# Optimization experiments

Measured on AMD Instinct MI355X. Metric: run time of the kernel, lower is better.

## Reference

```python
import jax, jax.numpy as jnp
import numpy as np

B, N, H, L, V = 512, 48, 256, 64, 800  # trees, nodes/tree (chain), hidden, latent, vocab


def _build_structure():
    # Chain tree: nodes 0..N-1; edges per tree: 2i=(i->i+1), 2i+1=(i+1->i).
    # DFS order with reverse edges: forward steps t=0..N-2 (label 0), then backtrack (label 1).
    T = 2 * (N - 1)
    Et = 2 * (N - 1)
    eid = np.zeros(T, np.int32); pred = np.zeros(T, np.int32); pm = np.zeros(T, bool)
    vl = np.zeros(T, np.int32)
    in0 = np.zeros(T, np.int32); m0 = np.zeros(T, bool)
    in1 = np.zeros(T, np.int32); m1 = np.zeros(T, bool)
    lab = np.zeros(T, np.int32)
    for t in range(N - 1):  # forward: edge (t -> t+1)
        eid[t] = 2 * t
        if t > 0:
            pred[t], pm[t] = 2 * (t - 1), True  # line-graph pred (t-1 -> t)
        v = t + 1; vl[t] = v
        in0[t], m0[t] = 2 * (v - 1), True       # in-edge (v-1 -> v)
        if v < N - 1:
            in1[t], m1[t] = 2 * v + 1, True     # in-edge (v+1 -> v), m still zero here
        lab[t] = 0
    for k in range(N - 1):  # backtrack: edge (u -> u-1)
        t = N - 1 + k; u = N - 1 - k
        eid[t] = 2 * (u - 1) + 1
        if u < N - 1:
            pred[t], pm[t] = 2 * u + 1, True    # line-graph pred (u+1 -> u)
        v = u - 1; vl[t] = v
        if v > 0:
            in0[t], m0[t] = 2 * (v - 1), True
        in1[t], m1[t] = 2 * v + 1, True
        lab[t] = 1
    eoff = (np.arange(B, dtype=np.int32) * Et)[None, :]
    noff = (np.arange(B, dtype=np.int32) * N)[None, :]
    src_l = np.empty(Et, np.int32); dst_l = np.empty(Et, np.int32)
    for i in range(N - 1):
        src_l[2 * i], dst_l[2 * i] = i, i + 1
        src_l[2 * i + 1], dst_l[2 * i + 1] = i + 1, i
    d = dict(
        step_eid=eid[:, None] + eoff,
        step_pred=pred[:, None] + eoff,
        step_pmask=np.broadcast_to(pm[:, None], (T, B)).copy(),
        step_v=vl[:, None] + noff,
        step_in0=in0[:, None] + eoff,
        step_m0=np.broadcast_to(m0[:, None], (T, B)).copy(),
        step_in1=in1[:, None] + eoff,
        step_m1=np.broadcast_to(m1[:, None], (T, B)).copy(),
        step_label=lab,
        edge_src=(src_l[None, :] + (np.arange(B, dtype=np.int32) * N)[:, None]).reshape(-1),
        edge_dst=(dst_l[None, :] + (np.arange(B, dtype=np.int32) * N)[:, None]).reshape(-1),
        root_ids=np.arange(B, dtype=np.int32) * N,
    )
    return {k: jnp.asarray(v) for k, v in d.items()}


def setup_inputs() -> dict:
    key = jax.random.key(0)
    ks = jax.random.split(key, 20)
    lin = lambda k, i, o: jax.random.normal(k, (i, o), jnp.float32) * (1.0 / np.sqrt(i))
    inp = _build_structure()
    inp['wid'] = jax.random.randint(ks[0], (B * N,), 0, V)
    inp['tree_vec'] = jax.random.normal(ks[1], (B, L), jnp.float32)
    inp['embedding'] = jax.random.normal(ks[2], (V, H), jnp.float32) * 0.1
    inp['Wz'] = lin(ks[3], 2 * H, H); inp['bz'] = jnp.zeros((H,), jnp.float32)
    inp['Wr'] = lin(ks[4], H, H)                                   # no bias (W_r)
    inp['Ur'] = lin(ks[5], H, H); inp['br'] = jnp.zeros((H,), jnp.float32)
    inp['Wh'] = lin(ks[6], 2 * H, H); inp['bh'] = jnp.zeros((H,), jnp.float32)
    inp['W_w'] = lin(ks[7], H + L, H); inp['W_b'] = jnp.zeros((H,), jnp.float32)
    inp['U_w'] = lin(ks[8], 2 * H + L, H); inp['U_b'] = jnp.zeros((H,), jnp.float32)
    inp['Wo_w'] = lin(ks[9], H, V); inp['Wo_b'] = jnp.zeros((V,), jnp.float32)
    inp['Us_w'] = lin(ks[10], H, 1); inp['Us_b'] = jnp.zeros((1,), jnp.float32)
    inp['n_fwd'] = N - 1
    return inp


def reference(wid, tree_vec, embedding, Wz, bz, Wr, Ur, br, Wh, bh,
              W_w, W_b, U_w, U_b, Wo_w, Wo_b, Us_w, Us_b,
              edge_src, edge_dst, root_ids,
              step_eid, step_pred, step_pmask, step_v,
              step_in0, step_m0, step_in1, step_m1,
              step_label, n_fwd):
    Hd = embedding.shape[1]
    Bn, Ld = tree_vec.shape
    E = edge_src.shape[0]
    x = embedding[wid]          # [n_nodes, H]
    src_x = x[edge_src]         # [E, H]
    dst_x = x[edge_dst]

    def gru_step(carry, st):
        m, rm = carry
        e = st['eid']
        pm = st['pmask'][:, None]
        s = jnp.where(pm, m[st['pred']], 0.0)        # line-graph pull of m -> s
        arm = jnp.where(pm, rm[st['pred']], 0.0)     # pull of rm -> accum_rm
        sx = src_x[e]
        z = jax.nn.sigmoid(jnp.concatenate([sx, s], 1) @ Wz + bz)
        mt = jnp.tanh(jnp.concatenate([sx, arm], 1) @ Wh + bh)
        m_e = (1.0 - z) * s + z * mt
        r = jax.nn.sigmoid(dst_x[e] @ Wr + m_e @ Ur + br)
        m = m.at[e].set(m_e)
        rm = rm.at[e].set(r * m_e)
        # node pull: h[v] = sum of m over all in-edges of v
        h_v = jnp.where(st['m0'][:, None], m[st['in0']], 0.0) \
            + jnp.where(st['m1'][:, None], m[st['in1']], 0.0)
        return (m, rm), h_v

    xs = {'eid': step_eid, 'pred': step_pred, 'pmask': step_pmask,
          'in0': step_in0, 'm0': step_m0, 'in1': step_in1, 'm1': step_m1}
    init = (jnp.zeros((E, Hd), x.dtype), jnp.zeros((E, Hd), x.dtype))
    _, hs = jax.lax.scan(gru_step, init, xs)  # [T, B, H]

    T = step_eid.shape[0]
    x_v = x[step_v]                                   # [T, B, H]
    tv = jnp.broadcast_to(tree_vec, (T, Bn, Ld))
    h_root = jnp.zeros((1, Bn, Hd), x.dtype)
    x_root = x[root_ids][None]
    p_in = jnp.concatenate([
        jnp.concatenate([x_root, h_root, tree_vec[None]], -1),
        jnp.concatenate([x_v, hs, tv], -1)], 0).reshape((T + 1) * Bn, 2 * Hd + Ld)
    p_tgt = jnp.concatenate([
        jnp.repeat((1 - step_label).astype(jnp.float32), Bn),
        jnp.zeros((Bn,), jnp.float32)])

    q_in = jnp.concatenate([
        jnp.concatenate([h_root[0], tree_vec], -1)[None],
        jnp.concatenate([hs[:n_fwd], tv[:n_fwd]], -1)], 0).reshape((n_fwd + 1) * Bn, Hd + Ld)
    q_tgt = jnp.concatenate([wid[root_ids][None], wid[step_v[:n_fwd]]], 0).reshape(-1)

    q = jax.nn.relu(q_in @ W_w + W_b) @ Wo_w + Wo_b
    p = (jax.nn.relu(p_in @ U_w + U_b) @ Us_w + Us_b)[:, 0]

    nt = jnp.float32(Bn)
    p_loss = jnp.sum(jnp.maximum(p, 0.0) - p * p_tgt + jnp.log1p(jnp.exp(-jnp.abs(p)))) / nt
    logq = jax.nn.log_softmax(q, -1)
    q_loss = -jnp.sum(jnp.take_along_axis(logq, q_tgt[:, None], 1)) / nt
    p_acc = jnp.mean(((p > 0).astype(jnp.int32) == p_tgt.astype(jnp.int32)).astype(jnp.float32))
    q_acc = jnp.mean((jnp.argmax(q, 1) == q_tgt).astype(jnp.float32))
    return q_loss, p_loss, q_acc, p_acc
```

## Files before the change

### kernel.cpp

```cpp
#include <hip/hip_runtime.h>
#include <math.h>

#define NTREE 512
#define NNODE 48
#define HD 256
#define LD 64
#define VOC 800
#define TSTEP 94
#define NFWD 47

typedef __attribute__((ext_vector_type(8))) short s8v;
typedef __attribute__((ext_vector_type(4))) float f4v;

__device__ __forceinline__ float sigm(float x) { return 1.f / (1.f + expf(-x)); }
__device__ __forceinline__ float sigm_f(float x) {
    return __builtin_amdgcn_rcpf(1.f + __expf(-x));
}
__device__ __forceinline__ float tanh_f(float x) {
    return 1.f - 2.f * __builtin_amdgcn_rcpf(1.f + __expf(2.f * x));
}

__device__ __forceinline__ float bfu(unsigned short u) {
    union { unsigned int i; float f; } c; c.i = ((unsigned int)u) << 16; return c.f;
}
__device__ __forceinline__ unsigned short f2bf(float f) {
    union { float f; unsigned int u; } c; c.f = f;
    return (unsigned short)((c.u + 0x7fffu + ((c.u >> 16) & 1u)) >> 16);
}
__device__ __forceinline__ s8v frag(const unsigned short* p) {
    union { int4 i; s8v v; } u; u.i = *(const int4*)p; return u.v;
}
__device__ __forceinline__ s8v zfrag() {
    union { int4 i; s8v v; } u; u.i = make_int4(0, 0, 0, 0); return u.v;
}
__device__ __forceinline__ void pin(s8v& v) {
    asm volatile("" : "+v"(v));
}
__device__ __forceinline__ void bar_lgkm() {
    asm volatile("s_waitcnt lgkmcnt(0)\n\ts_barrier" ::: "memory");
}

#define PV 8
__global__ __launch_bounds__(256) void prep_xproj(
    const float* __restrict__ emb,
    const float* __restrict__ Wz, const float* __restrict__ bz,
    const float* __restrict__ Wh, const float* __restrict__ bh,
    const float* __restrict__ Wr, const float* __restrict__ br,
    float* __restrict__ xzT, float* __restrict__ xhT, float* __restrict__ xrT)
{
    __shared__ float embL[PV][HD];
    const int j = threadIdx.x;
    const int v0 = blockIdx.x * PV;
    for (int r = 0; r < PV; ++r) embL[r][j] = emb[(v0 + r) * HD + j];
    __syncthreads();

    float az[PV], ah[PV], ar[PV];
#pragma unroll
    for (int r = 0; r < PV; ++r) { az[r] = bz[j]; ah[r] = bh[j]; ar[r] = br[j]; }
    for (int i = 0; i < HD; i += 4) {
        float wz0 = Wz[(i + 0) * HD + j], wz1 = Wz[(i + 1) * HD + j];
        float wz2 = Wz[(i + 2) * HD + j], wz3 = Wz[(i + 3) * HD + j];
        float wh0 = Wh[(i + 0) * HD + j], wh1 = Wh[(i + 1) * HD + j];
        float wh2 = Wh[(i + 2) * HD + j], wh3 = Wh[(i + 3) * HD + j];
        float wr0 = Wr[(i + 0) * HD + j], wr1 = Wr[(i + 1) * HD + j];
        float wr2 = Wr[(i + 2) * HD + j], wr3 = Wr[(i + 3) * HD + j];
#pragma unroll
        for (int r = 0; r < PV; ++r) {
            float4 e = *(const float4*)&embL[r][i];
            az[r] += e.x * wz0 + e.y * wz1 + e.z * wz2 + e.w * wz3;
            ah[r] += e.x * wh0 + e.y * wh1 + e.z * wh2 + e.w * wh3;
            ar[r] += e.x * wr0 + e.y * wr1 + e.z * wr2 + e.w * wr3;
        }
    }
#pragma unroll
    for (int r = 0; r < PV; ++r) {
        xzT[(v0 + r) * HD + j] = az[r];
        xhT[(v0 + r) * HD + j] = ah[r];
        xrT[(v0 + r) * HD + j] = ar[r];
    }
}

__global__ __launch_bounds__(256) void tcvt3(
    const float* __restrict__ Wz, const float* __restrict__ Wh,
    const float* __restrict__ Ur,
    unsigned short* __restrict__ WzT, unsigned short* __restrict__ WhT,
    unsigned short* __restrict__ UrT)
{
    const int which = blockIdx.x >> 8, n = blockIdx.x & 255, k = threadIdx.x;
    const float* src = (which == 0) ? (Wz + HD * HD) : (which == 1) ? (Wh + HD * HD) : Ur;
    unsigned short* dst = (which == 0) ? WzT : (which == 1) ? WhT : UrT;
    dst[n * HD + k] = f2bf(src[k * HD + n]);
}

__global__ __launch_bounds__(256) void tcvtQ(
    const float* __restrict__ Ww, const float* __restrict__ Wow,
    const float* __restrict__ Uw,
    unsigned short* __restrict__ W1T, unsigned short* __restrict__ WoT,
    unsigned short* __restrict__ UwT)
{
    int b = blockIdx.x;
    if (b < 256) {
        for (int k = threadIdx.x; k < 320; k += 256)
            W1T[b * 320 + k] = f2bf(Ww[k * 256 + b]);
    } else if (b < 1056) {
        int n = b - 256;
        WoT[n * 256 + threadIdx.x] = f2bf(Wow[threadIdx.x * VOC + n]);
    } else {
        int n = b - 1056;
        for (int k = threadIdx.x; k < 576; k += 256)
            UwT[n * 576 + k] = f2bf(Uw[k * 256 + n]);
    }
}

__global__ __launch_bounds__(256) void cvtE(
    const float* __restrict__ emb, const float* __restrict__ tv,
    unsigned short* __restrict__ embB, unsigned short* __restrict__ tvB)
{
    int idx = blockIdx.x * 256 + threadIdx.x;
    if (idx < VOC * HD) embB[idx] = f2bf(emb[idx]);
    else {
        int i2 = idx - VOC * HD;
        if (i2 < NTREE * LD) tvB[i2] = f2bf(tv[i2]);
    }
}

__global__ __launch_bounds__(512, 2) void gru10(
    const int* __restrict__ wid,
    const float* __restrict__ xzT, const float* __restrict__ xhT,
    const float* __restrict__ xrT,
    const unsigned short* __restrict__ WzT, const unsigned short* __restrict__ WhT,
    const unsigned short* __restrict__ UrT,
    unsigned short* __restrict__ hsb)
{
    __shared__ unsigned short urL[16 * 8 * 64 * 8];
    __shared__ unsigned short mBL[2][2][HD], armBL[2][2][HD];
    __shared__ int widL[2][NNODE];

    const int tid = threadIdx.x;
    const int wave = tid >> 6, lane = tid & 63;
    const int lq = lane >> 4, ln = lane & 15;
    const int b0 = blockIdx.x * 2;
    const int T0 = 2 * wave, T1 = T0 + 1;
    const int ftree = lane >> 5;
    const int fcol  = wave * 32 + (lane & 31);
    const int srcl  = lane & 15;
    const bool hi16 = (lane & 16) != 0;
    const bool hi32 = (lane & 32) != 0;

    if (tid < 2 * NNODE) widL[tid / NNODE][tid % NNODE] =
        wid[(b0 + tid / NNODE) * NNODE + (tid % NNODE)];

#pragma unroll
    for (int s = 0; s < 16; ++s) {
        *(int4*)&urL[((s * 8 + wave) * 64 + lane) * 8] =
            *(const int4*)&UrT[(s * 16 + ln) * HD + wave * 32 + lq * 8];
    }

    s8v wz0[8], wz1[8], wh0[8], wh1[8];
#pragma unroll
    for (int kt = 0; kt < 8; ++kt) {
        const int ko = kt * 32 + lq * 8;
        wz0[kt] = frag(&WzT[(T0 * 16 + ln) * HD + ko]);
        wz1[kt] = frag(&WzT[(T1 * 16 + ln) * HD + ko]);
        wh0[kt] = frag(&WhT[(T0 * 16 + ln) * HD + ko]);
        wh1[kt] = frag(&WhT[(T1 * 16 + ln) * HD + ko]);
    }
#pragma unroll
    for (int kt = 0; kt < 8; ++kt) {
        pin(wz0[kt]); pin(wz1[kt]); pin(wh0[kt]); pin(wh1[kt]);
    }
    __syncthreads();

    float cxz, cxh, cxr, chsp = 0.f, me = 0.f;
    float nxz = 0.f, nxh = 0.f, nxr = 0.f, nhsp = 0.f;
    {
        const int ws = widL[ftree][0], wd = widL[ftree][1];
        cxz = xzT[ws * HD + fcol];
        cxh = xhT[ws * HD + fcol];
        cxr = xrT[wd * HD + fcol];
    }

#pragma unroll 2
    for (int t = 0; t < TSTEP; ++t) {
        const int par = t & 1, nxt = par ^ 1;
        const bool fwd = t < NFWD;
        const bool hp = (t != 0) && (t != NFWD);

        {
            if (t == NFWD)
                chsp = bfu(hsb[((NFWD - 2) * NTREE + b0 + ftree) * HD + fcol]);
            const int tn = t + 1;
            if (tn < TSTEP) {
                const bool fwdn = tn < NFWD;
                const int un = TSTEP - tn;
                const int srcn = fwdn ? tn : un;
                const int dstn = fwdn ? (tn + 1) : (un - 1);
                const int ws = widL[ftree][srcn], wd = widL[ftree][dstn];
                nxz = xzT[ws * HD + fcol];
                nxh = xhT[ws * HD + fcol];
                nxr = xrT[wd * HD + fcol];
                nhsp = 0.f;
                if (tn > NFWD && dstn > 0)
                    nhsp = bfu(hsb[((dstn - 1) * NTREE + b0 + ftree) * HD + fcol]);
            }
        }

        float az = 0.f, ah = 0.f;
        if (hp) {
            f4v cz0 = (f4v){0.f,0.f,0.f,0.f}, cz1 = cz0, ch0 = cz0, ch1 = cz0;
#pragma unroll
            for (int kt = 0; kt < 8; ++kt) {
                const int ko = kt * 32 + lq * 8;
                s8v am = (ln < 2) ? frag(&mBL[par][ln][ko]) : zfrag();
                s8v aa = (ln < 2) ? frag(&armBL[par][ln][ko]) : zfrag();
                cz0 = __builtin_amdgcn_mfma_f32_16x16x32_bf16(am, wz0[kt], cz0, 0, 0, 0);
                cz1 = __builtin_amdgcn_mfma_f32_16x16x32_bf16(am, wz1[kt], cz1, 0, 0, 0);
                ch0 = __builtin_amdgcn_mfma_f32_16x16x32_bf16(aa, wh0[kt], ch0, 0, 0, 0);
                ch1 = __builtin_amdgcn_mfma_f32_16x16x32_bf16(aa, wh1[kt], ch1, 0, 0, 0);
            }
            float a00 = __shfl(cz0[0], srcl), a01 = __shfl(cz0[1], srcl);
            float a10 = __shfl(cz1[0], srcl), a11 = __shfl(cz1[1], srcl);
            az = hi16 ? (hi32 ? a11 : a10) : (hi32 ? a01 : a00);
            float h00 = __shfl(ch0[0], srcl), h01 = __shfl(ch0[1], srcl);
            float h10 = __shfl(ch1[0], srcl), h11 = __shfl(ch1[1], srcl);
            ah = hi16 ? (hi32 ? h11 : h10) : (hi32 ? h01 : h00);
        }

        {
            float azv = cxz, ahv = cxh, sold = 0.f;
            if (hp) { azv += az; ahv += ah; sold = me; }
            float z = sigm_f(azv), mt = tanh_f(ahv);
            me = sold + z * (mt - sold);
            float hv = fwd ? me : (me + chsp);
            hsb[(t * NTREE + b0 + ftree) * HD + fcol] = f2bf(hv);
            mBL[nxt][ftree][fcol] = f2bf(me);
        }
        bar_lgkm();

        {
            f4v cr0 = (f4v){0.f,0.f,0.f,0.f}, cr1 = cr0;
#pragma unroll
            for (int kt = 0; kt < 8; ++kt) {
                const int ko = kt * 32 + lq * 8;
                s8v a = (ln < 2) ? frag(&mBL[nxt][ln][ko]) : zfrag();
                s8v b0f = frag(&urL[((T0 * 8 + kt) * 64 + lane) * 8]);
                s8v b1f = frag(&urL[((T1 * 8 + kt) * 64 + lane) * 8]);
                cr0 = __builtin_amdgcn_mfma_f32_16x16x32_bf16(a, b0f, cr0, 0, 0, 0);
                cr1 = __builtin_amdgcn_mfma_f32_16x16x32_bf16(a, b1f, cr1, 0, 0, 0);
            }
            float r00 = __shfl(cr0[0], srcl), r01 = __shfl(cr0[1], srcl);
            float r10 = __shfl(cr1[0], srcl), r11 = __shfl(cr1[1], srcl);
            float ar = hi16 ? (hi32 ? r11 : r10) : (hi32 ? r01 : r00);
            float r = sigm_f(cxr + ar);
            armBL[nxt][ftree][fcol] = f2bf(r * me);
            cxz = nxz; cxh = nxh; cxr = nxr; chsp = nhsp;
        }
        bar_lgkm();
    }
}

#define QG 32
#define PG 32
struct QSmem {
    unsigned short X1L[QG][328];
    unsigned short hidL[QG][264];
    int tgts[QG];
    float wred[4][QG][4];
};
struct PSmem {
    unsigned short XL[PG][584];
    int widL[PG];
    float wredp[4][PG];
};

__global__ __launch_bounds__(256) void heads(
    const int* __restrict__ wid,
    const unsigned short* __restrict__ tvB,
    const unsigned short* __restrict__ embB,
    const unsigned short* __restrict__ hsb,
    const unsigned short* __restrict__ W1T,
    const unsigned short* __restrict__ WoT,
    const unsigned short* __restrict__ UwT,
    const float* __restrict__ Wb, const float* __restrict__ Wob,
    const float* __restrict__ Ub,
    const float* __restrict__ Usw, const float* __restrict__ Usb,
    float* __restrict__ acc)
{
    __shared__ __align__(16) char smem[sizeof(QSmem) > sizeof(PSmem) ? sizeof(QSmem) : sizeof(PSmem)];
    const int tid = threadIdx.x;
    const int wave = tid >> 6, lane = tid & 63;
    const int lq = lane >> 4, ln = lane & 15;

    if (blockIdx.x < 768) {
        QSmem& S = *(QSmem*)smem;
        const int trow = blockIdx.x >> 4;
        const int b0 = (blockIdx.x & 15) * QG;

        if (tid < QG) S.tgts[tid] = wid[(b0 + tid) * NNODE + trow];
        if (trow == 0) {
            int4 z = make_int4(0, 0, 0, 0);
            for (int idx = tid; idx < QG * 32; idx += 256) {
                int m = idx >> 5, c = idx & 31;
                *(int4*)&S.X1L[m][c * 8] = z;
            }
        } else {
            const unsigned short* hrow = hsb + (size_t)(trow - 1) * NTREE * HD;
            for (int idx = tid; idx < QG * 32; idx += 256) {
                int m = idx >> 5, c = idx & 31;
                *(int4*)&S.X1L[m][c * 8] = *(const int4*)&hrow[(b0 + m) * HD + c * 8];
            }
        }
        for (int idx = tid; idx < QG * 8; idx += 256) {
            int m = idx >> 3, c = idx & 7;
            *(int4*)&S.X1L[m][256 + c * 8] = *(const int4*)&tvB[(b0 + m) * LD + c * 8];
        }
        __syncthreads();

        f4v acc1[2][4];
#pragma unroll
        for (int mt = 0; mt < 2; ++mt)
#pragma unroll
            for (int nt = 0; nt < 4; ++nt) acc1[mt][nt] = (f4v){0.f, 0.f, 0.f, 0.f};
#pragma unroll
        for (int kt = 0; kt < 10; ++kt) {
            s8v a0 = frag(&S.X1L[ln][kt * 32 + lq * 8]);
            s8v a1 = frag(&S.X1L[16 + ln][kt * 32 + lq * 8]);
#pragma unroll
            for (int nt = 0; nt < 4; ++nt) {
                int n = wave * 64 + nt * 16 + ln;
                s8v b = frag(&W1T[n * 320 + kt * 32 + lq * 8]);
                acc1[0][nt] = __builtin_amdgcn_mfma_f32_16x16x32_bf16(a0, b, acc1[0][nt], 0, 0, 0);
                acc1[1][nt] = __builtin_amdgcn_mfma_f32_16x16x32_bf16(a1, b, acc1[1][nt], 0, 0, 0);
            }
        }
#pragma unroll
        for (int nt = 0; nt < 4; ++nt) {
            int col = wave * 64 + nt * 16 + ln;
            float wb = Wb[col];
#pragma unroll
            for (int mt = 0; mt < 2; ++mt)
#pragma unroll
                for (int r = 0; r < 4; ++r)
                    S.hidL[mt * 16 + lq * 4 + r][col] = f2bf(fmaxf(acc1[mt][nt][r] + wb, 0.f));
        }
        __syncthreads();

        int rt[2][4];
#pragma unroll
        for (int mt = 0; mt < 2; ++mt)
#pragma unroll
            for (int r = 0; r < 4; ++r) rt[mt][r] = S.tgts[mt * 16 + lq * 4 + r];
        float mx[2][4], ls[2][4], tg[2][4]; int am[2][4];
#pragma unroll
        for (int mt = 0; mt < 2; ++mt)
#pragma unroll
            for (int r = 0; r < 4; ++r) { mx[mt][r] = -1e30f; ls[mt][r] = 0.f; tg[mt][r] = 0.f; am[mt][r] = 1 << 30; }

        for (int nt = wave; nt < 50; nt += 4) {
            int n = nt * 16 + ln;
            const unsigned short* wrow = WoT + n * 256;
            f4v a2[2];
            a2[0] = (f4v){0.f, 0.f, 0.f, 0.f}; a2[1] = (f4v){0.f, 0.f, 0.f, 0.f};
#pragma unroll
            for (int kt = 0; kt < 8; ++kt) {
                s8v a0 = frag(&S.hidL[ln][kt * 32 + lq * 8]);
                s8v a1 = frag(&S.hidL[16 + ln][kt * 32 + lq * 8]);
                s8v b = frag(&wrow[kt * 32 + lq * 8]);
                a2[0] = __builtin_amdgcn_mfma_f32_16x16x32_bf16(a0, b, a2[0], 0, 0, 0);
                a2[1] = __builtin_amdgcn_mfma_f32_16x16x32_bf16(a1, b, a2[1], 0, 0, 0);
            }
            float bias = Wob[n];
#pragma unroll
            for (int mt = 0; mt < 2; ++mt)
#pragma unroll
                for (int r = 0; r < 4; ++r) {
                    float v = a2[mt][r] + bias;
                    if (n == rt[mt][r]) tg[mt][r] = v;
                    float nm = fmaxf(mx[mt][r], v);
                    ls[mt][r] = ls[mt][r] * __expf(mx[mt][r] - nm) + __expf(v - nm);
                    if (v > mx[mt][r]) am[mt][r] = n;
                    mx[mt][r] = nm;
                }
        }

#pragma unroll
        for (int s = 1; s < 16; s <<= 1) {
#pragma unroll
            for (int mt = 0; mt < 2; ++mt)
#pragma unroll
                for (int r = 0; r < 4; ++r) {
                    float mo = __shfl_xor(mx[mt][r], s);
                    float lo = __shfl_xor(ls[mt][r], s);
                    int   ao = __shfl_xor(am[mt][r], s);
                    float to = __shfl_xor(tg[mt][r], s);
                    tg[mt][r] += to;
                    float nm = fmaxf(mx[mt][r], mo);
                    ls[mt][r] = ls[mt][r] * __expf(mx[mt][r] - nm) + lo * __expf(mo - nm);
                    if (mo > mx[mt][r] || (mo == mx[mt][r] && ao < am[mt][r])) am[mt][r] = ao;
                    mx[mt][r] = nm;
                }
        }
        if (ln == 0) {
#pragma unroll
            for (int mt = 0; mt < 2; ++mt)
#pragma unroll
                for (int r = 0; r < 4; ++r) {
                    int row = mt * 16 + lq * 4 + r;
                    S.wred[wave][row][0] = mx[mt][r];
                    S.wred[wave][row][1] = ls[mt][r];
                    S.wred[wave][row][2] = __int_as_float(am[mt][r]);
                    S.wred[wave][row][3] = tg[mt][r];
                }
        }
        __syncthreads();

        float lossv = 0.f, corrv = 0.f;
        if (tid < QG) {
            float m_ = -1e30f, l_ = 0.f, t_ = 0.f; int a_ = 1 << 30;
#pragma unroll
            for (int w = 0; w < 4; ++w) {
                float mo = S.wred[w][tid][0], lo = S.wred[w][tid][1], to = S.wred[w][tid][3];
                int ao = __float_as_int(S.wred[w][tid][2]);
                t_ += to;
                float nm = fmaxf(m_, mo);
                l_ = l_ * __expf(m_ - nm) + lo * __expf(mo - nm);
                if (mo > m_ || (mo == m_ && ao < a_)) a_ = ao;
                m_ = nm;
            }
            lossv = m_ + logf(l_) - t_;
            corrv = (a_ == S.tgts[tid]) ? 1.f : 0.f;
        }
        if (wave == 0) {
            for (int s = 32; s; s >>= 1) {
                lossv += __shfl_down(lossv, s);
                corrv += __shfl_down(corrv, s);
            }
            if (tid == 0) {
                int slot = blockIdx.x & 255;
                atomicAdd(&acc[0 * 256 + slot], lossv);
                atomicAdd(&acc[2 * 256 + slot], corrv);
            }
        }
    } else {
        PSmem& S = *(PSmem*)smem;
        const int pb = blockIdx.x - 768;
        const int trow = pb >> 4;
        const int b0 = (pb & 15) * PG;
        const int node = (trow == 0) ? 0 : ((trow <= NFWD) ? trow : (TSTEP - trow));

        if (tid < PG) S.widL[tid] = wid[(b0 + tid) * NNODE + node];
        __syncthreads();

        for (int idx = tid; idx < PG * 32; idx += 256) {
            int m = idx >> 5, c = idx & 31;
            *(int4*)&S.XL[m][c * 8] = *(const int4*)&embB[S.widL[m] * HD + c * 8];
        }
        if (trow == 0) {
            int4 z = make_int4(0, 0, 0, 0);
            for (int idx = tid; idx < PG * 32; idx += 256) {
                int m = idx >> 5, c = idx & 31;
                *(int4*)&S.XL[m][256 + c * 8] = z;
            }
        } else {
            const unsigned short* hrow = hsb + (size_t)(trow - 1) * NTREE * HD;
            for (int idx = tid; idx < PG * 32; idx += 256) {
                int m = idx >> 5, c = idx & 31;
                *(int4*)&S.XL[m][256 + c * 8] = *(const int4*)&hrow[(b0 + m) * HD + c * 8];
            }
        }
        for (int idx = tid; idx < PG * 8; idx += 256) {
            int m = idx >> 3, c = idx & 7;
            *(int4*)&S.XL[m][512 + c * 8] = *(const int4*)&tvB[(b0 + m) * LD + c * 8];
        }
        __syncthreads();

        f4v a1[2][4];
#pragma unroll
        for (int mt = 0; mt < 2; ++mt)
#pragma unroll
            for (int nt = 0; nt < 4; ++nt) a1[mt][nt] = (f4v){0.f, 0.f, 0.f, 0.f};
        for (int kt = 0; kt < 18; ++kt) {
            s8v a0 = frag(&S.XL[ln][kt * 32 + lq * 8]);
            s8v am_ = frag(&S.XL[16 + ln][kt * 32 + lq * 8]);
#pragma unroll
            for (int nt = 0; nt < 4; ++nt) {
                int n = wave * 64 + nt * 16 + ln;
                s8v b = frag(&UwT[n * 576 + kt * 32 + lq * 8]);
                a1[0][nt] = __builtin_amdgcn_mfma_f32_16x16x32_bf16(a0, b, a1[0][nt], 0, 0, 0);
                a1[1][nt] = __builtin_amdgcn_mfma_f32_16x16x32_bf16(am_, b, a1[1][nt], 0, 0, 0);
            }
        }
        float part[2][4] = {{0, 0, 0, 0}, {0, 0, 0, 0}};
#pragma unroll
        for (int nt = 0; nt < 4; ++nt) {
            int n = wave * 64 + nt * 16 + ln;
            float ub = Ub[n], us = Usw[n];
#pragma unroll
            for (int mt = 0; mt < 2; ++mt)
#pragma unroll
                for (int r = 0; r < 4; ++r)
                    part[mt][r] += fmaxf(a1[mt][nt][r] + ub, 0.f) * us;
        }
#pragma unroll
        for (int s = 1; s < 16; s <<= 1) {
#pragma unroll
            for (int mt = 0; mt < 2; ++mt)
#pragma unroll
                for (int r = 0; r < 4; ++r)
                    part[mt][r] += __shfl_xor(part[mt][r], s);
        }
        if (ln == 0) {
#pragma unroll
            for (int mt = 0; mt < 2; ++mt)
#pragma unroll
                for (int r = 0; r < 4; ++r)
                    S.wredp[wave][mt * 16 + lq * 4 + r] = part[mt][r];
        }
        __syncthreads();

        float lossv = 0.f, corrv = 0.f;
        if (tid < PG) {
            float p = S.wredp[0][tid] + S.wredp[1][tid] + S.wredp[2][tid] + S.wredp[3][tid] + Usb[0];
            float tgt = (trow < NFWD) ? 1.f : 0.f;
            lossv = fmaxf(p, 0.f) - p * tgt + log1pf(expf(-fabsf(p)));
            corrv = (((p > 0.f) ? 1 : 0) == ((trow < NFWD) ? 1 : 0)) ? 1.f : 0.f;
        }
        if (wave == 0) {
            for (int s = 32; s; s >>= 1) {
                lossv += __shfl_down(lossv, s);
                corrv += __shfl_down(corrv, s);
            }
            if (tid == 0) {
                int slot = blockIdx.x & 255;
                atomicAdd(&acc[1 * 256 + slot], lossv);
                atomicAdd(&acc[3 * 256 + slot], corrv);
            }
        }
    }
}

__global__ void init_kernel(float* __restrict__ acc) {
    acc[threadIdx.x] = 0.f;
}

__global__ void fin_kernel(const float* __restrict__ acc, float* __restrict__ out) {
    const int tid = threadIdx.x;
    const int c = tid >> 6, lane = tid & 63;
    float v = 0.f;
    for (int i = lane; i < 256; i += 64) v += acc[c * 256 + i];
    for (int s = 32; s; s >>= 1) v += __shfl_down(v, s);
    if (lane == 0) {
        const float sc[4] = {1.f / 512.f, 1.f / 512.f, 1.f / 24576.f, 1.f / 48640.f};
        out[c] = v * sc[c];
    }
}

extern "C" void kernel_launch(void* const* d_in, const int* in_sizes, int n_in,
                              void* d_out, int out_size, void* d_ws, size_t ws_size,
                              hipStream_t stream) {
    const int*   wid  = (const int*)  d_in[12];
    const float* tv   = (const float*)d_in[13];
    const float* emb  = (const float*)d_in[14];
    const float* Wz   = (const float*)d_in[15];
    const float* bz   = (const float*)d_in[16];
    const float* Wr   = (const float*)d_in[17];
    const float* Ur   = (const float*)d_in[18];
    const float* br   = (const float*)d_in[19];
    const float* Wh   = (const float*)d_in[20];
    const float* bh   = (const float*)d_in[21];
    const float* Ww   = (const float*)d_in[22];
    const float* Wb   = (const float*)d_in[23];
    const float* Uw   = (const float*)d_in[24];
    const float* Ubias= (const float*)d_in[25];
    const float* Wow  = (const float*)d_in[26];
    const float* Wob  = (const float*)d_in[27];
    const float* Usw  = (const float*)d_in[28];
    const float* Usb  = (const float*)d_in[29];

    char* w = (char*)d_ws;
    float* accb = (float*)w;
    float* xzT  = (float*)(w + 4096);
    float* xhT  = (float*)(w + 823296);
    float* xrT  = (float*)(w + 1642496);
    unsigned short* WzT2 = (unsigned short*)(w + 2461696);
    unsigned short* WhT2 = (unsigned short*)(w + 2592768);
    unsigned short* UrT2 = (unsigned short*)(w + 2723840);
    unsigned short* hsb  = (unsigned short*)(w + 2854912);
    unsigned short* W1T  = (unsigned short*)(w + 27496448);
    unsigned short* WoT  = (unsigned short*)(w + 27660288);
    unsigned short* UwT  = (unsigned short*)(w + 28069888);
    unsigned short* embB = (unsigned short*)(w + 28364800);
    unsigned short* tvB  = (unsigned short*)(w + 28774400);

    init_kernel<<<1, 1024, 0, stream>>>(accb);
    prep_xproj<<<VOC / PV, 256, 0, stream>>>(emb, Wz, bz, Wh, bh, Wr, br, xzT, xhT, xrT);
    tcvt3<<<768, 256, 0, stream>>>(Wz, Wh, Ur, WzT2, WhT2, UrT2);
    tcvtQ<<<1312, 256, 0, stream>>>(Ww, Wow, Uw, W1T, WoT, UwT);
    cvtE<<<(VOC * HD + NTREE * LD + 255) / 256, 256, 0, stream>>>(emb, tv, embB, tvB);
    gru10<<<NTREE / 2, 512, 0, stream>>>(wid, xzT, xhT, xrT, WzT2, WhT2, UrT2, hsb);
    heads<<<768 + 1520, 256, 0, stream>>>(wid, tvB, embB, hsb, W1T, WoT, UwT,
                                          Wb, Wob, Ubias, Usw, Usb, accb);
    fin_kernel<<<1, 256, 0, stream>>>(accb, (float*)d_out);
}
```

Baseline: 455.3 us.

## Merge prep kernels, split MFMA accumulator chains, load head operands directly

```diff
diff --git a/kernel.cpp b/kernel.cpp
--- a/kernel.cpp
+++ b/kernel.cpp
@@ -12,7 +12,6 @@
 typedef __attribute__((ext_vector_type(8))) short s8v;
 typedef __attribute__((ext_vector_type(4))) float f4v;
 
-__device__ __forceinline__ float sigm(float x) { return 1.f / (1.f + expf(-x)); }
 __device__ __forceinline__ float sigm_f(float x) {
     return __builtin_amdgcn_rcpf(1.f + __expf(-x));
 }
@@ -32,9 +31,6 @@
 }
 __device__ __forceinline__ s8v zfrag() {
     union { int4 i; s8v v; } u; u.i = make_int4(0, 0, 0, 0); return u.v;
-}
-__device__ __forceinline__ void pin(s8v& v) {
-    asm volatile("" : "+v"(v));
 }
 __device__ __forceinline__ void bar_lgkm() {
     asm volatile("s_waitcnt lgkmcnt(0)\n\ts_barrier" ::: "memory");
@@ -80,51 +76,52 @@
     }
 }
 
-__global__ __launch_bounds__(256) void tcvt3(
+__global__ __launch_bounds__(256) void prep_misc(
     const float* __restrict__ Wz, const float* __restrict__ Wh,
     const float* __restrict__ Ur,
-    unsigned short* __restrict__ WzT, unsigned short* __restrict__ WhT,
-    unsigned short* __restrict__ UrT)
-{
-    const int which = blockIdx.x >> 8, n = blockIdx.x & 255, k = threadIdx.x;
-    const float* src = (which == 0) ? (Wz + HD * HD) : (which == 1) ? (Wh + HD * HD) : Ur;
-    unsigned short* dst = (which == 0) ? WzT : (which == 1) ? WhT : UrT;
-    dst[n * HD + k] = f2bf(src[k * HD + n]);
-}
-
-__global__ __launch_bounds__(256) void tcvtQ(
     const float* __restrict__ Ww, const float* __restrict__ Wow,
     const float* __restrict__ Uw,
+    const float* __restrict__ emb, const float* __restrict__ tv,
+    unsigned short* __restrict__ WzT, unsigned short* __restrict__ WhT,
+    unsigned short* __restrict__ UrT,
     unsigned short* __restrict__ W1T, unsigned short* __restrict__ WoT,
-    unsigned short* __restrict__ UwT)
+    unsigned short* __restrict__ UwT,
+    unsigned short* __restrict__ embB, unsigned short* __restrict__ tvB,
+    float* __restrict__ acc)
 {
     int b = blockIdx.x;
-    if (b < 256) {
-        for (int k = threadIdx.x; k < 320; k += 256)
-            W1T[b * 320 + k] = f2bf(Ww[k * 256 + b]);
-    } else if (b < 1056) {
-        int n = b - 256;
-        WoT[n * 256 + threadIdx.x] = f2bf(Wow[threadIdx.x * VOC + n]);
+    if (b < 4) {
+        acc[b * 256 + threadIdx.x] = 0.f;
+    } else if (b < 772) {
+        int bb = b - 4;
+        const int which = bb >> 8, n = bb & 255, k = threadIdx.x;
+        const float* src = (which == 0) ? (Wz + HD * HD) : (which == 1) ? (Wh + HD * HD) : Ur;
+        unsigned short* dst = (which == 0) ? WzT : (which == 1) ? WhT : UrT;
+        dst[n * HD + k] = f2bf(src[k * HD + n]);
+    } else if (b < 2084) {
+        int bb = b - 772;
+        if (bb < 256) {
+            for (int k = threadIdx.x; k < 320; k += 256)
+                W1T[bb * 320 + k] = f2bf(Ww[k * 256 + bb]);
+        } else if (bb < 1056) {
+            int n = bb - 256;
+            WoT[n * 256 + threadIdx.x] = f2bf(Wow[threadIdx.x * VOC + n]);
+        } else {
+            int n = bb - 1056;
+            for (int k = threadIdx.x; k < 576; k += 256)
+                UwT[n * 576 + k] = f2bf(Uw[k * 256 + n]);
+        }
     } else {
-        int n = b - 1056;
-        for (int k = threadIdx.x; k < 576; k += 256)
-            UwT[n * 576 + k] = f2bf(Uw[k * 256 + n]);
-    }
-}
-
-__global__ __launch_bounds__(256) void cvtE(
-    const float* __restrict__ emb, const float* __restrict__ tv,
-    unsigned short* __restrict__ embB, unsigned short* __restrict__ tvB)
-{
-    int idx = blockIdx.x * 256 + threadIdx.x;
-    if (idx < VOC * HD) embB[idx] = f2bf(emb[idx]);
-    else {
-        int i2 = idx - VOC * HD;
-        if (i2 < NTREE * LD) tvB[i2] = f2bf(tv[i2]);
-    }
-}
-
-__global__ __launch_bounds__(512, 2) void gru10(
+        int idx = (b - 2084) * 256 + threadIdx.x;
+        if (idx < VOC * HD) embB[idx] = f2bf(emb[idx]);
+        else {
+            int i2 = idx - VOC * HD;
+            if (i2 < NTREE * LD) tvB[i2] = f2bf(tv[i2]);
+        }
+    }
+}
+
+__global__ __launch_bounds__(512, 2) void gru11(
     const int* __restrict__ wid,
     const float* __restrict__ xzT, const float* __restrict__ xhT,
     const float* __restrict__ xrT,
@@ -164,10 +161,6 @@
         wz1[kt] = frag(&WzT[(T1 * 16 + ln) * HD + ko]);
         wh0[kt] = frag(&WhT[(T0 * 16 + ln) * HD + ko]);
         wh1[kt] = frag(&WhT[(T1 * 16 + ln) * HD + ko]);
-    }
-#pragma unroll
-    for (int kt = 0; kt < 8; ++kt) {
-        pin(wz0[kt]); pin(wz1[kt]); pin(wh0[kt]); pin(wh1[kt]);
     }
     __syncthreads();
 
@@ -207,17 +200,30 @@
 
         float az = 0.f, ah = 0.f;
         if (hp) {
-            f4v cz0 = (f4v){0.f,0.f,0.f,0.f}, cz1 = cz0, ch0 = cz0, ch1 = cz0;
-#pragma unroll
-            for (int kt = 0; kt < 8; ++kt) {
+            f4v cz0a = (f4v){0.f,0.f,0.f,0.f}, cz0b = cz0a, cz1a = cz0a, cz1b = cz0a;
+            f4v ch0a = cz0a, ch0b = cz0a, ch1a = cz0a, ch1b = cz0a;
+#pragma unroll
+            for (int kt = 0; kt < 4; ++kt) {
                 const int ko = kt * 32 + lq * 8;
                 s8v am = (ln < 2) ? frag(&mBL[par][ln][ko]) : zfrag();
                 s8v aa = (ln < 2) ? frag(&armBL[par][ln][ko]) : zfrag();
-                cz0 = __builtin_amdgcn_mfma_f32_16x16x32_bf16(am, wz0[kt], cz0, 0, 0, 0);
-                cz1 = __builtin_amdgcn_mfma_f32_16x16x32_bf16(am, wz1[kt], cz1, 0, 0, 0);
-                ch0 = __builtin_amdgcn_mfma_f32_16x16x32_bf16(aa, wh0[kt], ch0, 0, 0, 0);
-                ch1 = __builtin_amdgcn_mfma_f32_16x16x32_bf16(aa, wh1[kt], ch1, 0, 0, 0);
-            }
+                cz0a = __builtin_amdgcn_mfma_f32_16x16x32_bf16(am, wz0[kt], cz0a, 0, 0, 0);
+                cz1a = __builtin_amdgcn_mfma_f32_16x16x32_bf16(am, wz1[kt], cz1a, 0, 0, 0);
+                ch0a = __builtin_amdgcn_mfma_f32_16x16x32_bf16(aa, wh0[kt], ch0a, 0, 0, 0);
+                ch1a = __builtin_amdgcn_mfma_f32_16x16x32_bf16(aa, wh1[kt], ch1a, 0, 0, 0);
+            }
+#pragma unroll
+            for (int kt = 4; kt < 8; ++kt) {
+                const int ko = kt * 32 + lq * 8;
+                s8v am = (ln < 2) ? frag(&mBL[par][ln][ko]) : zfrag();
+                s8v aa = (ln < 2) ? frag(&armBL[par][ln][ko]) : zfrag();
+                cz0b = __builtin_amdgcn_mfma_f32_16x16x32_bf16(am, wz0[kt], cz0b, 0, 0, 0);
+                cz1b = __builtin_amdgcn_mfma_f32_16x16x32_bf16(am, wz1[kt], cz1b, 0, 0, 0);
+                ch0b = __builtin_amdgcn_mfma_f32_16x16x32_bf16(aa, wh0[kt], ch0b, 0, 0, 0);
+                ch1b = __builtin_amdgcn_mfma_f32_16x16x32_bf16(aa, wh1[kt], ch1b, 0, 0, 0);
+            }
+            f4v cz0 = cz0a + cz0b, cz1 = cz1a + cz1b;
+            f4v ch0 = ch0a + ch0b, ch1 = ch1a + ch1b;
             float a00 = __shfl(cz0[0], srcl), a01 = __shfl(cz0[1], srcl);
             float a10 = __shfl(cz1[0], srcl), a11 = __shfl(cz1[1], srcl);
             az = hi16 ? (hi32 ? a11 : a10) : (hi32 ? a01 : a00);
@@ -238,16 +244,26 @@
         bar_lgkm();
 
         {
-            f4v cr0 = (f4v){0.f,0.f,0.f,0.f}, cr1 = cr0;
-#pragma unroll
-            for (int kt = 0; kt < 8; ++kt) {
+            f4v cr0a = (f4v){0.f,0.f,0.f,0.f}, cr0b = cr0a, cr1a = cr0a, cr1b = cr0a;
+#pragma unroll
+            for (int kt = 0; kt < 4; ++kt) {
                 const int ko = kt * 32 + lq * 8;
                 s8v a = (ln < 2) ? frag(&mBL[nxt][ln][ko]) : zfrag();
                 s8v b0f = frag(&urL[((T0 * 8 + kt) * 64 + lane) * 8]);
                 s8v b1f = frag(&urL[((T1 * 8 + kt) * 64 + lane) * 8]);
-                cr0 = __builtin_amdgcn_mfma_f32_16x16x32_bf16(a, b0f, cr0, 0, 0, 0);
-                cr1 = __builtin_amdgcn_mfma_f32_16x16x32_bf16(a, b1f, cr1, 0, 0, 0);
-            }
+                cr0a = __builtin_amdgcn_mfma_f32_16x16x32_bf16(a, b0f, cr0a, 0, 0, 0);
+                cr1a = __builtin_amdgcn_mfma_f32_16x16x32_bf16(a, b1f, cr1a, 0, 0, 0);
+            }
+#pragma unroll
+            for (int kt = 4; kt < 8; ++kt) {
+                const int ko = kt * 32 + lq * 8;
+                s8v a = (ln < 2) ? frag(&mBL[nxt][ln][ko]) : zfrag();
+                s8v b0f = frag(&urL[((T0 * 8 + kt) * 64 + lane) * 8]);
+                s8v b1f = frag(&urL[((T1 * 8 + kt) * 64 + lane) * 8]);
+                cr0b = __builtin_amdgcn_mfma_f32_16x16x32_bf16(a, b0f, cr0b, 0, 0, 0);
+                cr1b = __builtin_amdgcn_mfma_f32_16x16x32_bf16(a, b1f, cr1b, 0, 0, 0);
+            }
+            f4v cr0 = cr0a + cr0b, cr1 = cr1a + cr1b;
             float r00 = __shfl(cr0[0], srcl), r01 = __shfl(cr0[1], srcl);
             float r10 = __shfl(cr1[0], srcl), r11 = __shfl(cr1[1], srcl);
             float ar = hi16 ? (hi32 ? r11 : r10) : (hi32 ? r01 : r00);
@@ -262,13 +278,11 @@
 #define QG 32
 #define PG 32
 struct QSmem {
-    unsigned short X1L[QG][328];
     unsigned short hidL[QG][264];
     int tgts[QG];
     float wred[4][QG][4];
 };
 struct PSmem {
-    unsigned short XL[PG][584];
     int widL[PG];
     float wredp[4][PG];
 };
@@ -297,34 +311,26 @@
         const int b0 = (blockIdx.x & 15) * QG;
 
         if (tid < QG) S.tgts[tid] = wid[(b0 + tid) * NNODE + trow];
-        if (trow == 0) {
-            int4 z = make_int4(0, 0, 0, 0);
-            for (int idx = tid; idx < QG * 32; idx += 256) {
-                int m = idx >> 5, c = idx & 31;
-                *(int4*)&S.X1L[m][c * 8] = z;
-            }
-        } else {
-            const unsigned short* hrow = hsb + (size_t)(trow - 1) * NTREE * HD;
-            for (int idx = tid; idx < QG * 32; idx += 256) {
-                int m = idx >> 5, c = idx & 31;
-                *(int4*)&S.X1L[m][c * 8] = *(const int4*)&hrow[(b0 + m) * HD + c * 8];
-            }
-        }
-        for (int idx = tid; idx < QG * 8; idx += 256) {
-            int m = idx >> 3, c = idx & 7;
-            *(int4*)&S.X1L[m][256 + c * 8] = *(const int4*)&tvB[(b0 + m) * LD + c * 8];
-        }
-        __syncthreads();
 
         f4v acc1[2][4];
 #pragma unroll
         for (int mt = 0; mt < 2; ++mt)
 #pragma unroll
             for (int nt = 0; nt < 4; ++nt) acc1[mt][nt] = (f4v){0.f, 0.f, 0.f, 0.f};
+        const unsigned short* hrow = hsb + (size_t)(trow - 1) * NTREE * HD;
 #pragma unroll
         for (int kt = 0; kt < 10; ++kt) {
-            s8v a0 = frag(&S.X1L[ln][kt * 32 + lq * 8]);
-            s8v a1 = frag(&S.X1L[16 + ln][kt * 32 + lq * 8]);
+            s8v a0, a1;
+            if (kt < 8) {
+                if (trow == 0) { a0 = zfrag(); a1 = zfrag(); }
+                else {
+                    a0 = frag(&hrow[(b0 + ln) * HD + kt * 32 + lq * 8]);
+                    a1 = frag(&hrow[(b0 + 16 + ln) * HD + kt * 32 + lq * 8]);
+                }
+            } else {
+                a0 = frag(&tvB[(b0 + ln) * LD + (kt - 8) * 32 + lq * 8]);
+                a1 = frag(&tvB[(b0 + 16 + ln) * LD + (kt - 8) * 32 + lq * 8]);
+            }
 #pragma unroll
             for (int nt = 0; nt < 4; ++nt) {
                 int n = wave * 64 + nt * 16 + ln;
@@ -345,6 +351,13 @@
         }
         __syncthreads();
 
+        s8v ha0[8], ha1[8];
+#pragma unroll
+        for (int kt = 0; kt < 8; ++kt) {
+            ha0[kt] = frag(&S.hidL[ln][kt * 32 + lq * 8]);
+            ha1[kt] = frag(&S.hidL[16 + ln][kt * 32 + lq * 8]);
+        }
+
         int rt[2][4];
 #pragma unroll
         for (int mt = 0; mt < 2; ++mt)
@@ -363,11 +376,9 @@
             a2[0] = (f4v){0.f, 0.f, 0.f, 0.f}; a2[1] = (f4v){0.f, 0.f, 0.f, 0.f};
 #pragma unroll
             for (int kt = 0; kt < 8; ++kt) {
-                s8v a0 = frag(&S.hidL[ln][kt * 32 + lq * 8]);
-                s8v a1 = frag(&S.hidL[16 + ln][kt * 32 + lq * 8]);
                 s8v b = frag(&wrow[kt * 32 + lq * 8]);
-                a2[0] = __builtin_amdgcn_mfma_f32_16x16x32_bf16(a0, b, a2[0], 0, 0, 0);
-                a2[1] = __builtin_amdgcn_mfma_f32_16x16x32_bf16(a1, b, a2[1], 0, 0, 0);
+                a2[0] = __builtin_amdgcn_mfma_f32_16x16x32_bf16(ha0[kt], b, a2[0], 0, 0, 0);
+                a2[1] = __builtin_amdgcn_mfma_f32_16x16x32_bf16(ha1[kt], b, a2[1], 0, 0, 0);
             }
             float bias = Wob[n];
 #pragma unroll
@@ -376,10 +387,11 @@
                 for (int r = 0; r < 4; ++r) {
                     float v = a2[mt][r] + bias;
                     if (n == rt[mt][r]) tg[mt][r] = v;
-                    float nm = fmaxf(mx[mt][r], v);
-                    ls[mt][r] = ls[mt][r] * __expf(mx[mt][r] - nm) + __expf(v - nm);
-                    if (v > mx[mt][r]) am[mt][r] = n;
-                    mx[mt][r] = nm;
+                    float d = v - mx[mt][r];
+                    float e = __expf(-fabsf(d));
+                    bool newmax = d > 0.f;
+                    ls[mt][r] = fmaf(ls[mt][r], newmax ? e : 1.f, newmax ? 1.f : e);
+                    if (newmax) { mx[mt][r] = v; am[mt][r] = n; }
                 }
         }
 
@@ -450,38 +462,30 @@
 
         if (tid < PG) S.widL[tid] = wid[(b0 + tid) * NNODE + node];
         __syncthreads();
-
-        for (int idx = tid; idx < PG * 32; idx += 256) {
-            int m = idx >> 5, c = idx & 31;
-            *(int4*)&S.XL[m][c * 8] = *(const int4*)&embB[S.widL[m] * HD + c * 8];
-        }
-        if (trow == 0) {
-            int4 z = make_int4(0, 0, 0, 0);
-            for (int idx = tid; idx < PG * 32; idx += 256) {
-                int m = idx >> 5, c = idx & 31;
-                *(int4*)&S.XL[m][256 + c * 8] = z;
-            }
-        } else {
-            const unsigned short* hrow = hsb + (size_t)(trow - 1) * NTREE * HD;
-            for (int idx = tid; idx < PG * 32; idx += 256) {
-                int m = idx >> 5, c = idx & 31;
-                *(int4*)&S.XL[m][256 + c * 8] = *(const int4*)&hrow[(b0 + m) * HD + c * 8];
-            }
-        }
-        for (int idx = tid; idx < PG * 8; idx += 256) {
-            int m = idx >> 3, c = idx & 7;
-            *(int4*)&S.XL[m][512 + c * 8] = *(const int4*)&tvB[(b0 + m) * LD + c * 8];
-        }
-        __syncthreads();
+        const int w0 = S.widL[ln], w1 = S.widL[16 + ln];
+        const unsigned short* hrow = hsb + (size_t)(trow - 1) * NTREE * HD;
 
         f4v a1[2][4];
 #pragma unroll
         for (int mt = 0; mt < 2; ++mt)
 #pragma unroll
             for (int nt = 0; nt < 4; ++nt) a1[mt][nt] = (f4v){0.f, 0.f, 0.f, 0.f};
+#pragma unroll 2
         for (int kt = 0; kt < 18; ++kt) {
-            s8v a0 = frag(&S.XL[ln][kt * 32 + lq * 8]);
-            s8v am_ = frag(&S.XL[16 + ln][kt * 32 + lq * 8]);
+            s8v a0, am_;
+            if (kt < 8) {
+                a0  = frag(&embB[w0 * HD + kt * 32 + lq * 8]);
+                am_ = frag(&embB[w1 * HD + kt * 32 + lq * 8]);
+            } else if (kt < 16) {
+                if (trow == 0) { a0 = zfrag(); am_ = zfrag(); }
+                else {
+                    a0  = frag(&hrow[(b0 + ln) * HD + (kt - 8) * 32 + lq * 8]);
+                    am_ = frag(&hrow[(b0 + 16 + ln) * HD + (kt - 8) * 32 + lq * 8]);
+                }
+            } else {
+                a0  = frag(&tvB[(b0 + ln) * LD + (kt - 16) * 32 + lq * 8]);
+                am_ = frag(&tvB[(b0 + 16 + ln) * LD + (kt - 16) * 32 + lq * 8]);
+            }
 #pragma unroll
             for (int nt = 0; nt < 4; ++nt) {
                 int n = wave * 64 + nt * 16 + ln;
@@ -537,10 +541,6 @@
             }
         }
     }
-}
-
-__global__ void init_kernel(float* __restrict__ acc) {
-    acc[threadIdx.x] = 0.f;
 }
 
 __global__ void fin_kernel(const float* __restrict__ acc, float* __restrict__ out) {
@@ -592,12 +592,11 @@
     unsigned short* embB = (unsigned short*)(w + 28364800);
     unsigned short* tvB  = (unsigned short*)(w + 28774400);
 
-    init_kernel<<<1, 1024, 0, stream>>>(accb);
     prep_xproj<<<VOC / PV, 256, 0, stream>>>(emb, Wz, bz, Wh, bh, Wr, br, xzT, xhT, xrT);
-    tcvt3<<<768, 256, 0, stream>>>(Wz, Wh, Ur, WzT2, WhT2, UrT2);
-    tcvtQ<<<1312, 256, 0, stream>>>(Ww, Wow, Uw, W1T, WoT, UwT);
-    cvtE<<<(VOC * HD + NTREE * LD + 255) / 256, 256, 0, stream>>>(emb, tv, embB, tvB);
-    gru10<<<NTREE / 2, 512, 0, stream>>>(wid, xzT, xhT, xrT, WzT2, WhT2, UrT2, hsb);
+    prep_misc<<<2084 + 513, 256, 0, stream>>>(Wz, Wh, Ur, Ww, Wow, Uw, emb, tv,
+                                              WzT2, WhT2, UrT2, W1T, WoT, UwT,
+                                              embB, tvB, accb);
+    gru11<<<NTREE / 2, 512, 0, stream>>>(wid, xzT, xhT, xrT, WzT2, WhT2, UrT2, hsb);
     heads<<<768 + 1520, 256, 0, stream>>>(wid, tvB, embB, hsb, W1T, WoT, UwT,
                                           Wb, Wob, Ubias, Usw, Usb, accb);
     fin_kernel<<<1, 256, 0, stream>>>(accb, (float*)d_out);
```

After: 489.1 us. 7.4% more time.

## Merge prep kernels, hoist head A-fragments, streamline online softmax, drop register pins

Applied to the files above, without the earlier changes.

```diff
diff --git a/kernel.cpp b/kernel.cpp
--- a/kernel.cpp
+++ b/kernel.cpp
@@ -12,7 +12,6 @@
 typedef __attribute__((ext_vector_type(8))) short s8v;
 typedef __attribute__((ext_vector_type(4))) float f4v;
 
-__device__ __forceinline__ float sigm(float x) { return 1.f / (1.f + expf(-x)); }
 __device__ __forceinline__ float sigm_f(float x) {
     return __builtin_amdgcn_rcpf(1.f + __expf(-x));
 }
@@ -32,9 +31,6 @@
 }
 __device__ __forceinline__ s8v zfrag() {
     union { int4 i; s8v v; } u; u.i = make_int4(0, 0, 0, 0); return u.v;
-}
-__device__ __forceinline__ void pin(s8v& v) {
-    asm volatile("" : "+v"(v));
 }
 __device__ __forceinline__ void bar_lgkm() {
     asm volatile("s_waitcnt lgkmcnt(0)\n\ts_barrier" ::: "memory");
@@ -80,47 +76,48 @@
     }
 }
 
-__global__ __launch_bounds__(256) void tcvt3(
+__global__ __launch_bounds__(256) void prep_misc(
     const float* __restrict__ Wz, const float* __restrict__ Wh,
     const float* __restrict__ Ur,
-    unsigned short* __restrict__ WzT, unsigned short* __restrict__ WhT,
-    unsigned short* __restrict__ UrT)
-{
-    const int which = blockIdx.x >> 8, n = blockIdx.x & 255, k = threadIdx.x;
-    const float* src = (which == 0) ? (Wz + HD * HD) : (which == 1) ? (Wh + HD * HD) : Ur;
-    unsigned short* dst = (which == 0) ? WzT : (which == 1) ? WhT : UrT;
-    dst[n * HD + k] = f2bf(src[k * HD + n]);
-}
-
-__global__ __launch_bounds__(256) void tcvtQ(
     const float* __restrict__ Ww, const float* __restrict__ Wow,
     const float* __restrict__ Uw,
+    const float* __restrict__ emb, const float* __restrict__ tv,
+    unsigned short* __restrict__ WzT, unsigned short* __restrict__ WhT,
+    unsigned short* __restrict__ UrT,
     unsigned short* __restrict__ W1T, unsigned short* __restrict__ WoT,
-    unsigned short* __restrict__ UwT)
+    unsigned short* __restrict__ UwT,
+    unsigned short* __restrict__ embB, unsigned short* __restrict__ tvB,
+    float* __restrict__ acc)
 {
     int b = blockIdx.x;
-    if (b < 256) {
-        for (int k = threadIdx.x; k < 320; k += 256)
-            W1T[b * 320 + k] = f2bf(Ww[k * 256 + b]);
-    } else if (b < 1056) {
-        int n = b - 256;
-        WoT[n * 256 + threadIdx.x] = f2bf(Wow[threadIdx.x * VOC + n]);
+    if (b < 4) {
+        acc[b * 256 + threadIdx.x] = 0.f;
+    } else if (b < 772) {
+        int bb = b - 4;
+        const int which = bb >> 8, n = bb & 255, k = threadIdx.x;
+        const float* src = (which == 0) ? (Wz + HD * HD) : (which == 1) ? (Wh + HD * HD) : Ur;
+        unsigned short* dst = (which == 0) ? WzT : (which == 1) ? WhT : UrT;
+        dst[n * HD + k] = f2bf(src[k * HD + n]);
+    } else if (b < 2084) {
+        int bb = b - 772;
+        if (bb < 256) {
+            for (int k = threadIdx.x; k < 320; k += 256)
+                W1T[bb * 320 + k] = f2bf(Ww[k * 256 + bb]);
+        } else if (bb < 1056) {
+            int n = bb - 256;
+            WoT[n * 256 + threadIdx.x] = f2bf(Wow[threadIdx.x * VOC + n]);
+        } else {
+            int n = bb - 1056;
+            for (int k = threadIdx.x; k < 576; k += 256)
+                UwT[n * 576 + k] = f2bf(Uw[k * 256 + n]);
+        }
     } else {
-        int n = b - 1056;
-        for (int k = threadIdx.x; k < 576; k += 256)
-            UwT[n * 576 + k] = f2bf(Uw[k * 256 + n]);
-    }
-}
-
-__global__ __launch_bounds__(256) void cvtE(
-    const float* __restrict__ emb, const float* __restrict__ tv,
-    unsigned short* __restrict__ embB, unsigned short* __restrict__ tvB)
-{
-    int idx = blockIdx.x * 256 + threadIdx.x;
-    if (idx < VOC * HD) embB[idx] = f2bf(emb[idx]);
-    else {
-        int i2 = idx - VOC * HD;
-        if (i2 < NTREE * LD) tvB[i2] = f2bf(tv[i2]);
+        int idx = (b - 2084) * 256 + threadIdx.x;
+        if (idx < VOC * HD) embB[idx] = f2bf(emb[idx]);
+        else {
+            int i2 = idx - VOC * HD;
+            if (i2 < NTREE * LD) tvB[i2] = f2bf(tv[i2]);
+        }
     }
 }
 
@@ -164,10 +161,6 @@
         wz1[kt] = frag(&WzT[(T1 * 16 + ln) * HD + ko]);
         wh0[kt] = frag(&WhT[(T0 * 16 + ln) * HD + ko]);
         wh1[kt] = frag(&WhT[(T1 * 16 + ln) * HD + ko]);
-    }
-#pragma unroll
-    for (int kt = 0; kt < 8; ++kt) {
-        pin(wz0[kt]); pin(wz1[kt]); pin(wh0[kt]); pin(wh1[kt]);
     }
     __syncthreads();
 
@@ -345,6 +338,13 @@
         }
         __syncthreads();
 
+        s8v ha0[8], ha1[8];
+#pragma unroll
+        for (int kt = 0; kt < 8; ++kt) {
+            ha0[kt] = frag(&S.hidL[ln][kt * 32 + lq * 8]);
+            ha1[kt] = frag(&S.hidL[16 + ln][kt * 32 + lq * 8]);
+        }
+
         int rt[2][4];
 #pragma unroll
         for (int mt = 0; mt < 2; ++mt)
@@ -363,11 +363,9 @@
             a2[0] = (f4v){0.f, 0.f, 0.f, 0.f}; a2[1] = (f4v){0.f, 0.f, 0.f, 0.f};
 #pragma unroll
             for (int kt = 0; kt < 8; ++kt) {
-                s8v a0 = frag(&S.hidL[ln][kt * 32 + lq * 8]);
-                s8v a1 = frag(&S.hidL[16 + ln][kt * 32 + lq * 8]);
                 s8v b = frag(&wrow[kt * 32 + lq * 8]);
-                a2[0] = __builtin_amdgcn_mfma_f32_16x16x32_bf16(a0, b, a2[0], 0, 0, 0);
-                a2[1] = __builtin_amdgcn_mfma_f32_16x16x32_bf16(a1, b, a2[1], 0, 0, 0);
+                a2[0] = __builtin_amdgcn_mfma_f32_16x16x32_bf16(ha0[kt], b, a2[0], 0, 0, 0);
+                a2[1] = __builtin_amdgcn_mfma_f32_16x16x32_bf16(ha1[kt], b, a2[1], 0, 0, 0);
             }
             float bias = Wob[n];
 #pragma unroll
@@ -376,10 +374,11 @@
                 for (int r = 0; r < 4; ++r) {
                     float v = a2[mt][r] + bias;
                     if (n == rt[mt][r]) tg[mt][r] = v;
-                    float nm = fmaxf(mx[mt][r], v);
-                    ls[mt][r] = ls[mt][r] * __expf(mx[mt][r] - nm) + __expf(v - nm);
-                    if (v > mx[mt][r]) am[mt][r] = n;
-                    mx[mt][r] = nm;
+                    float d = v - mx[mt][r];
+                    float e = __expf(-fabsf(d));
+                    bool newmax = d > 0.f;
+                    ls[mt][r] = fmaf(ls[mt][r], newmax ? e : 1.f, newmax ? 1.f : e);
+                    if (newmax) { mx[mt][r] = v; am[mt][r] = n; }
                 }
         }
 
@@ -537,10 +536,6 @@
             }
         }
     }
-}
-
-__global__ void init_kernel(float* __restrict__ acc) {
-    acc[threadIdx.x] = 0.f;
 }
 
 __global__ void fin_kernel(const float* __restrict__ acc, float* __restrict__ out) {
@@ -592,11 +587,10 @@
     unsigned short* embB = (unsigned short*)(w + 28364800);
     unsigned short* tvB  = (unsigned short*)(w + 28774400);
 
-    init_kernel<<<1, 1024, 0, stream>>>(accb);
     prep_xproj<<<VOC / PV, 256, 0, stream>>>(emb, Wz, bz, Wh, bh, Wr, br, xzT, xhT, xrT);
-    tcvt3<<<768, 256, 0, stream>>>(Wz, Wh, Ur, WzT2, WhT2, UrT2);
-    tcvtQ<<<1312, 256, 0, stream>>>(Ww, Wow, Uw, W1T, WoT, UwT);
-    cvtE<<<(VOC * HD + NTREE * LD + 255) / 256, 256, 0, stream>>>(emb, tv, embB, tvB);
+    prep_misc<<<3012, 256, 0, stream>>>(Wz, Wh, Ur, Ww, Wow, Uw, emb, tv,
+                                        WzT2, WhT2, UrT2, W1T, WoT, UwT,
+                                        embB, tvB, accb);
     gru10<<<NTREE / 2, 512, 0, stream>>>(wid, xzT, xhT, xrT, WzT2, WhT2, UrT2, hsb);
     heads<<<768 + 1520, 256, 0, stream>>>(wid, tvB, embB, hsb, W1T, WoT, UwT,
                                           Wb, Wob, Ubias, Usw, Usb, accb);
```

After: 448.1 us (median of 2 runs). About the same (-1.6%).
